# Performance work log

Measured on AMD Instinct MI355X. Metric: run time of the kernel, lower is better.

Reference implementation:

```python
import jax, jax.numpy as jnp
import numpy as np

EMBED_DIM = 1024
B, S = 8, 4096

def setup_inputs() -> dict:
    key = jax.random.key(0)
    k_x, k_w1, k_b1, k_phi, k_w2, k_b2 = jax.random.split(key, 6)
    lim1 = 1.0 / np.sqrt(EMBED_DIM)
    lim2 = 1.0  # linear2 fan_in = ffn_dim = 1
    return {
        "x": jax.random.normal(k_x, (B, S, EMBED_DIM), dtype=jnp.float32),
        "W1": jax.random.uniform(k_w1, (1, EMBED_DIM), jnp.float32, -lim1, lim1),
        "b1": jax.random.uniform(k_b1, (1,), jnp.float32, -lim1, lim1),
        "phi": jax.random.uniform(k_phi, (), jnp.float32, 0.0, 2.0 * np.pi),
        "W2": jax.random.uniform(k_w2, (EMBED_DIM, 1), jnp.float32, -lim2, lim2),
        "b2": jax.random.uniform(k_b2, (EMBED_DIM,), jnp.float32, -lim2, lim2),
    }

def reference(x, W1, b1, phi, W2, b2):
    # linear1: per-token projection to a scalar angle theta  [B,S,1]
    theta = jnp.einsum("bsd,od->bso", x, W1) + b1
    # 1-qubit circuit RY(theta) -> RX(phi) -> <PauliZ> on |0>
    # closed form: <Z> = cos(theta) * cos(phi)
    q = jnp.cos(theta) * jnp.cos(phi)  # [B,S,1]
    # dropout=0 (eval); linear2: ffn_dim(=1) -> embed_dim
    out = jnp.einsum("bso,do->bsd", q, W2) + b2  # [B,S,EMBED_DIM]
    return out
```

## Files before the change

kernel.cpp:

```cpp
#include <hip/hip_runtime.h>
#include <math.h>


#define EMBED_D 1024
#define NTOK    (8 * 4096)

__global__ __launch_bounds__(256) void ffq_kernel(
    const float* __restrict__ x,
    const float* __restrict__ W1,
    const float* __restrict__ b1,
    const float* __restrict__ phi,
    const float* __restrict__ W2,
    const float* __restrict__ b2,
    float* __restrict__ out,
    int ntok)
{
    const int lane  = threadIdx.x & 63;
    const int wib   = threadIdx.x >> 6;
    const int gwave = blockIdx.x * 4 + wib;
    const int nwav  = gridDim.x * 4;

    float4 w1r[4], w2r[4], b2r[4];
    const float4* w14 = (const float4*)W1;
    const float4* w24 = (const float4*)W2;
    const float4* b24 = (const float4*)b2;
    #pragma unroll
    for (int c = 0; c < 4; ++c) {
        w1r[c] = w14[c * 64 + lane];
        w2r[c] = w24[c * 64 + lane];
        b2r[c] = b24[c * 64 + lane];
    }
    const float cphi = cosf(phi[0]);
    const float b1v  = b1[0];

    for (int tok = gwave; tok < ntok; tok += nwav) {
        const float4* x4 = (const float4*)(x + (size_t)tok * EMBED_D);

        float4 xv[4];
        #pragma unroll
        for (int c = 0; c < 4; ++c) xv[c] = x4[c * 64 + lane];

        float v = 0.f;
        #pragma unroll
        for (int c = 0; c < 4; ++c) {
            v = fmaf(xv[c].x, w1r[c].x, v);
            v = fmaf(xv[c].y, w1r[c].y, v);
            v = fmaf(xv[c].z, w1r[c].z, v);
            v = fmaf(xv[c].w, w1r[c].w, v);
        }

        #pragma unroll
        for (int m = 32; m > 0; m >>= 1)
            v += __shfl_xor(v, m, 64);

        const float q = cosf(v + b1v) * cphi;

        float4* o4 = (float4*)(out + (size_t)tok * EMBED_D);
        #pragma unroll
        for (int c = 0; c < 4; ++c) {
            float4 o;
            o.x = fmaf(q, w2r[c].x, b2r[c].x);
            o.y = fmaf(q, w2r[c].y, b2r[c].y);
            o.z = fmaf(q, w2r[c].z, b2r[c].z);
            o.w = fmaf(q, w2r[c].w, b2r[c].w);
            o4[c * 64 + lane] = o;
        }
    }
}

extern "C" void kernel_launch(void* const* d_in, const int* in_sizes, int n_in,
                              void* d_out, int out_size, void* d_ws, size_t ws_size,
                              hipStream_t stream) {
    const float* x   = (const float*)d_in[0];
    const float* W1  = (const float*)d_in[1];
    const float* b1  = (const float*)d_in[2];
    const float* phi = (const float*)d_in[3];
    const float* W2  = (const float*)d_in[4];
    const float* b2  = (const float*)d_in[5];
    float* out = (float*)d_out;

    const int ntok = NTOK;

    ffq_kernel<<<2048, 256, 0, stream>>>(x, W1, b1, phi, W2, b2, out, ntok);
}
```

Baseline: 239.9 us.

## Batch four tokens per wave with upfront loads and nontemporal stores

```diff
diff --git a/kernel.cpp b/kernel.cpp
--- a/kernel.cpp
+++ b/kernel.cpp
@@ -4,6 +4,10 @@
 
 #define EMBED_D 1024
 #define NTOK    (8 * 4096)
+#define TPW     4
+#define TOK_PER_BLOCK (4 * TPW)
+
+typedef float f4 __attribute__((ext_vector_type(4)));
 
 __global__ __launch_bounds__(256) void ffq_kernel(
     const float* __restrict__ x,
@@ -12,18 +16,24 @@
     const float* __restrict__ phi,
     const float* __restrict__ W2,
     const float* __restrict__ b2,
-    float* __restrict__ out,
-    int ntok)
+    float* __restrict__ out)
 {
-    const int lane  = threadIdx.x & 63;
-    const int wib   = threadIdx.x >> 6;
-    const int gwave = blockIdx.x * 4 + wib;
-    const int nwav  = gridDim.x * 4;
+    const int lane = threadIdx.x & 63;
+    const int wib  = threadIdx.x >> 6;
+    const int tok0 = (blockIdx.x * 4 + wib) * TPW;
 
-    float4 w1r[4], w2r[4], b2r[4];
-    const float4* w14 = (const float4*)W1;
-    const float4* w24 = (const float4*)W2;
-    const float4* b24 = (const float4*)b2;
+    const f4* xb = (const f4*)x + (size_t)tok0 * (EMBED_D / 4);
+    f4 xv[TPW][4];
+    #pragma unroll
+    for (int t = 0; t < TPW; ++t)
+        #pragma unroll
+        for (int c = 0; c < 4; ++c)
+            xv[t][c] = xb[t * (EMBED_D / 4) + c * 64 + lane];
+
+    const f4* w14 = (const f4*)W1;
+    const f4* w24 = (const f4*)W2;
+    const f4* b24 = (const f4*)b2;
+    f4 w1r[4], w2r[4], b2r[4];
     #pragma unroll
     for (int c = 0; c < 4; ++c) {
         w1r[c] = w14[c * 64 + lane];
@@ -33,37 +43,43 @@
     const float cphi = cosf(phi[0]);
     const float b1v  = b1[0];
 
-    for (int tok = gwave; tok < ntok; tok += nwav) {
-        const float4* x4 = (const float4*)(x + (size_t)tok * EMBED_D);
-
-        float4 xv[4];
-        #pragma unroll
-        for (int c = 0; c < 4; ++c) xv[c] = x4[c * 64 + lane];
-
-        float v = 0.f;
+    float v[TPW];
+    #pragma unroll
+    for (int t = 0; t < TPW; ++t) {
+        float s = 0.f;
         #pragma unroll
         for (int c = 0; c < 4; ++c) {
-            v = fmaf(xv[c].x, w1r[c].x, v);
-            v = fmaf(xv[c].y, w1r[c].y, v);
-            v = fmaf(xv[c].z, w1r[c].z, v);
-            v = fmaf(xv[c].w, w1r[c].w, v);
+            s = fmaf(xv[t][c].x, w1r[c].x, s);
+            s = fmaf(xv[t][c].y, w1r[c].y, s);
+            s = fmaf(xv[t][c].z, w1r[c].z, s);
+            s = fmaf(xv[t][c].w, w1r[c].w, s);
         }
+        v[t] = s;
+    }
 
+    #pragma unroll
+    for (int m = 32; m > 0; m >>= 1) {
         #pragma unroll
-        for (int m = 32; m > 0; m >>= 1)
-            v += __shfl_xor(v, m, 64);
+        for (int t = 0; t < TPW; ++t)
+            v[t] += __shfl_xor(v[t], m, 64);
+    }
 
-        const float q = cosf(v + b1v) * cphi;
+    float q[TPW];
+    #pragma unroll
+    for (int t = 0; t < TPW; ++t)
+        q[t] = cosf(v[t] + b1v) * cphi;
 
-        float4* o4 = (float4*)(out + (size_t)tok * EMBED_D);
+    f4* ob = (f4*)out + (size_t)tok0 * (EMBED_D / 4);
+    #pragma unroll
+    for (int t = 0; t < TPW; ++t) {
         #pragma unroll
         for (int c = 0; c < 4; ++c) {
-            float4 o;
-            o.x = fmaf(q, w2r[c].x, b2r[c].x);
-            o.y = fmaf(q, w2r[c].y, b2r[c].y);
-            o.z = fmaf(q, w2r[c].z, b2r[c].z);
-            o.w = fmaf(q, w2r[c].w, b2r[c].w);
-            o4[c * 64 + lane] = o;
+            f4 o;
+            o.x = fmaf(q[t], w2r[c].x, b2r[c].x);
+            o.y = fmaf(q[t], w2r[c].y, b2r[c].y);
+            o.z = fmaf(q[t], w2r[c].z, b2r[c].z);
+            o.w = fmaf(q[t], w2r[c].w, b2r[c].w);
+            __builtin_nontemporal_store(o, &ob[t * (EMBED_D / 4) + c * 64 + lane]);
         }
     }
 }
@@ -79,7 +95,5 @@
     const float* b2  = (const float*)d_in[5];
     float* out = (float*)d_out;
 
-    const int ntok = NTOK;
-
-    ffq_kernel<<<2048, 256, 0, stream>>>(x, W1, b1, phi, W2, b2, out, ntok);
+    ffq_kernel<<<NTOK / TOK_PER_BLOCK, 256, 0, stream>>>(x, W1, b1, phi, W2, b2, out);
 }
```

Result: slower. 245.9 us (+2.5%).

## Split fused kernel into theta-reduction and broadcast-write kernels with nontemporal stores

Applied to the files above, without the earlier changes.

```diff
diff --git a/kernel.cpp b/kernel.cpp
--- a/kernel.cpp
+++ b/kernel.cpp
@@ -5,66 +5,70 @@
 #define EMBED_D 1024
 #define NTOK    (8 * 4096)
 
-__global__ __launch_bounds__(256) void ffq_kernel(
+typedef float f4 __attribute__((ext_vector_type(4)));
+
+__global__ __launch_bounds__(256) void ffq_theta(
     const float* __restrict__ x,
     const float* __restrict__ W1,
     const float* __restrict__ b1,
     const float* __restrict__ phi,
+    float* __restrict__ q_ws)
+{
+    const int lane = threadIdx.x & 63;
+    const int wib  = threadIdx.x >> 6;
+    const int tok  = blockIdx.x * 4 + wib;
+
+    const f4* x4 = (const f4*)x + (size_t)tok * (EMBED_D / 4);
+    f4 xv[4];
+    #pragma unroll
+    for (int c = 0; c < 4; ++c) xv[c] = x4[c * 64 + lane];
+
+    const f4* w14 = (const f4*)W1;
+    f4 w1r[4];
+    #pragma unroll
+    for (int c = 0; c < 4; ++c) w1r[c] = w14[c * 64 + lane];
+
+    float s = 0.f;
+    #pragma unroll
+    for (int c = 0; c < 4; ++c) {
+        s = fmaf(xv[c].x, w1r[c].x, s);
+        s = fmaf(xv[c].y, w1r[c].y, s);
+        s = fmaf(xv[c].z, w1r[c].z, s);
+        s = fmaf(xv[c].w, w1r[c].w, s);
+    }
+
+    #pragma unroll
+    for (int m = 32; m > 0; m >>= 1)
+        s += __shfl_xor(s, m, 64);
+
+    if (lane == 0)
+        q_ws[tok] = cosf(s + b1[0]) * cosf(phi[0]);
+}
+
+__global__ __launch_bounds__(256) void ffq_out(
+    const float* __restrict__ q_ws,
     const float* __restrict__ W2,
     const float* __restrict__ b2,
-    float* __restrict__ out,
-    int ntok)
+    float* __restrict__ out)
 {
-    const int lane  = threadIdx.x & 63;
-    const int wib   = threadIdx.x >> 6;
-    const int gwave = blockIdx.x * 4 + wib;
-    const int nwav  = gridDim.x * 4;
+    const int t = threadIdx.x;
+    const int b = blockIdx.x;
 
-    float4 w1r[4], w2r[4], b2r[4];
-    const float4* w14 = (const float4*)W1;
-    const float4* w24 = (const float4*)W2;
-    const float4* b24 = (const float4*)b2;
+    const f4 qv  = ((const f4*)q_ws)[b];
+    const f4 w2v = ((const f4*)W2)[t];
+    const f4 b2v = ((const f4*)b2)[t];
+
+    f4* ob = (f4*)out + (size_t)b * 4 * (EMBED_D / 4);
+    const float qq[4] = { qv.x, qv.y, qv.z, qv.w };
+
     #pragma unroll
-    for (int c = 0; c < 4; ++c) {
-        w1r[c] = w14[c * 64 + lane];
-        w2r[c] = w24[c * 64 + lane];
-        b2r[c] = b24[c * 64 + lane];
-    }
-    const float cphi = cosf(phi[0]);
-    const float b1v  = b1[0];
-
-    for (int tok = gwave; tok < ntok; tok += nwav) {
-        const float4* x4 = (const float4*)(x + (size_t)tok * EMBED_D);
-
-        float4 xv[4];
-        #pragma unroll
-        for (int c = 0; c < 4; ++c) xv[c] = x4[c * 64 + lane];
-
-        float v = 0.f;
-        #pragma unroll
-        for (int c = 0; c < 4; ++c) {
-            v = fmaf(xv[c].x, w1r[c].x, v);
-            v = fmaf(xv[c].y, w1r[c].y, v);
-            v = fmaf(xv[c].z, w1r[c].z, v);
-            v = fmaf(xv[c].w, w1r[c].w, v);
-        }
-
-        #pragma unroll
-        for (int m = 32; m > 0; m >>= 1)
-            v += __shfl_xor(v, m, 64);
-
-        const float q = cosf(v + b1v) * cphi;
-
-        float4* o4 = (float4*)(out + (size_t)tok * EMBED_D);
-        #pragma unroll
-        for (int c = 0; c < 4; ++c) {
-            float4 o;
-            o.x = fmaf(q, w2r[c].x, b2r[c].x);
-            o.y = fmaf(q, w2r[c].y, b2r[c].y);
-            o.z = fmaf(q, w2r[c].z, b2r[c].z);
-            o.w = fmaf(q, w2r[c].w, b2r[c].w);
-            o4[c * 64 + lane] = o;
-        }
+    for (int tt = 0; tt < 4; ++tt) {
+        f4 o;
+        o.x = fmaf(qq[tt], w2v.x, b2v.x);
+        o.y = fmaf(qq[tt], w2v.y, b2v.y);
+        o.z = fmaf(qq[tt], w2v.z, b2v.z);
+        o.w = fmaf(qq[tt], w2v.w, b2v.w);
+        __builtin_nontemporal_store(o, &ob[tt * (EMBED_D / 4) + t]);
     }
 }
 
@@ -78,8 +82,8 @@
     const float* W2  = (const float*)d_in[4];
     const float* b2  = (const float*)d_in[5];
     float* out = (float*)d_out;
+    float* q_ws = (float*)d_ws;
 
-    const int ntok = NTOK;
-
-    ffq_kernel<<<2048, 256, 0, stream>>>(x, W1, b1, phi, W2, b2, out, ntok);
+    ffq_theta<<<NTOK / 4, 256, 0, stream>>>(x, W1, b1, phi, q_ws);
+    ffq_out<<<NTOK / 4, 256, 0, stream>>>(q_ws, W2, b2, out);
 }
```

Result: no change. 236.2 us (-1.6%).
